# Optimization experiments

Measured on AMD Instinct MI355X. Metric: run time of the kernel, lower is better.

Reference implementation:

```python
import jax, jax.numpy as jnp
import numpy as np

N_EMBD = 768
N_HEAD = 12
HEAD_DIM = N_EMBD // N_HEAD
B, T = 2, 2048
EPS = 1e-5


def setup_inputs() -> dict:
    key = jax.random.key(0)
    ks = jax.random.split(key, 16)
    s = 0.02
    return {
        "x": jax.random.normal(ks[0], (B, T, N_EMBD), dtype=jnp.float32),
        "ln1_g": jnp.ones((N_EMBD,), jnp.float32),
        "ln1_b": jnp.zeros((N_EMBD,), jnp.float32),
        "W_attn": jax.random.normal(ks[1], (N_EMBD, 3 * N_EMBD), jnp.float32) * s,
        "b_attn": jnp.zeros((3 * N_EMBD,), jnp.float32),
        "W_cproj": jax.random.normal(ks[2], (N_EMBD, N_EMBD), jnp.float32) * s,
        "b_cproj": jnp.zeros((N_EMBD,), jnp.float32),
        "ln2_g": jnp.ones((N_EMBD,), jnp.float32),
        "ln2_b": jnp.zeros((N_EMBD,), jnp.float32),
        "W_fc": jax.random.normal(ks[3], (N_EMBD, 4 * N_EMBD), jnp.float32) * s,
        "b_fc": jnp.zeros((4 * N_EMBD,), jnp.float32),
        "W_mproj": jax.random.normal(ks[4], (4 * N_EMBD, N_EMBD), jnp.float32) * s,
        "b_mproj": jnp.zeros((N_EMBD,), jnp.float32),
    }


def _layernorm(x, g, b):
    mu = jnp.mean(x, axis=-1, keepdims=True)
    var = jnp.mean(jnp.square(x - mu), axis=-1, keepdims=True)
    return (x - mu) * jax.lax.rsqrt(var + EPS) * g + b


def _attention(h, W_attn, b_attn, W_cproj, b_cproj):
    Bx, Tx, C = h.shape
    qkv = h @ W_attn + b_attn  # [B, T, 3C]
    q, k, v = jnp.split(qkv, 3, axis=-1)
    # [B, H, T, D]
    def split_heads(t):
        return t.reshape(Bx, Tx, N_HEAD, HEAD_DIM).transpose(0, 2, 1, 3)
    q, k, v = split_heads(q), split_heads(k), split_heads(v)
    att = jnp.einsum("bhqd,bhkd->bhqk", q, k) / np.sqrt(HEAD_DIM).astype(np.float32)
    causal = jnp.tril(jnp.ones((Tx, Tx), dtype=bool))
    att = jnp.where(causal, att, jnp.float32(-jnp.inf))
    att = jax.nn.softmax(att, axis=-1)
    y = jnp.einsum("bhqk,bhkd->bhqd", att, v)
    y = y.transpose(0, 2, 1, 3).reshape(Bx, Tx, C)
    return y @ W_cproj + b_cproj


def _mlp(h, W_fc, b_fc, W_mproj, b_mproj):
    return jax.nn.gelu(h @ W_fc + b_fc, approximate=False) @ W_mproj + b_mproj


def reference(x, ln1_g, ln1_b, W_attn, b_attn, W_cproj, b_cproj,
              ln2_g, ln2_b, W_fc, b_fc, W_mproj, b_mproj):
    x = x + _attention(_layernorm(x, ln1_g, ln1_b), W_attn, b_attn, W_cproj, b_cproj)
    x = x + _mlp(_layernorm(x, ln2_g, ln2_b), W_fc, b_fc, W_mproj, b_mproj)
    return x
```

## Files before the change

### kernel.cpp

```cpp
#include <hip/hip_runtime.h>
#include <cstdint>
#include <cstddef>

#define B_ 2
#define T_ 2048
#define C_ 768
#define H_ 12
#define D_ 64

typedef __attribute__((ext_vector_type(8))) short s16x8;
typedef __attribute__((ext_vector_type(4))) float fx4;

static __device__ __forceinline__ unsigned short f2bf(float f) {
  unsigned u = __builtin_bit_cast(unsigned, f);
  unsigned r = u + 0x7fffu + ((u >> 16) & 1u);
  return (unsigned short)(r >> 16);
}
static __device__ __forceinline__ unsigned short f2bf_trunc(float f) {
  return (unsigned short)(__builtin_bit_cast(unsigned, f) >> 16);
}

static __device__ __forceinline__ void glds16(const unsigned short* g, unsigned short* l) {
  __builtin_amdgcn_global_load_lds(
      (const __attribute__((address_space(1))) void*)(g),
      (__attribute__((address_space(3))) void*)(l), 16, 0, 0);
}

__global__ __launch_bounds__(256) void prep(
    const float* __restrict__ Wattn, const float* __restrict__ Wcproj,
    const float* __restrict__ Wfc, const float* __restrict__ Wmproj,
    unsigned short* __restrict__ WattnT, unsigned short* __restrict__ WcprojT,
    unsigned short* __restrict__ WfcT, unsigned short* __restrict__ WmprojT,
    const float* __restrict__ X, const float* __restrict__ g,
    const float* __restrict__ bb, unsigned short* __restrict__ O) {
  __shared__ float tile[32][33];
  __shared__ float ps[8];
  int bid = blockIdx.x, tid = threadIdx.x;
  if (bid < 6912) {
    const float* W; unsigned short* Wt; int R, C, idx;
    if (bid < 1728)      { W = Wattn;  Wt = WattnT;  R = 768;  C = 2304; idx = bid; }
    else if (bid < 2304) { W = Wcproj; Wt = WcprojT; R = 768;  C = 768;  idx = bid - 1728; }
    else if (bid < 4608) { W = Wfc;    Wt = WfcT;    R = 768;  C = 3072; idx = bid - 2304; }
    else                 { W = Wmproj; Wt = WmprojT; R = 3072; C = 768;  idx = bid - 4608; }
    int ct = C >> 5;
    int c0 = (idx % ct) * 32, r0 = (idx / ct) * 32;
    int tx = tid & 31, ty = tid >> 5;
#pragma unroll
    for (int i = 0; i < 4; ++i)
      tile[ty + i * 8][tx] = W[(size_t)(r0 + ty + i * 8) * C + (c0 + tx)];
    __syncthreads();
#pragma unroll
    for (int i = 0; i < 4; ++i)
      Wt[(size_t)(c0 + ty + i * 8) * R + (r0 + tx)] = f2bf(tile[tx][ty + i * 8]);
  } else {
    int row = bid - 6912;
    const float* xr = X + (size_t)row * C_;
    float v0 = xr[tid], v1 = xr[tid + 256], v2 = xr[tid + 512];
    float s = v0 + v1 + v2;
    float s2 = v0 * v0 + v1 * v1 + v2 * v2;
#pragma unroll
    for (int off = 1; off < 64; off <<= 1) {
      s += __shfl_xor(s, off);
      s2 += __shfl_xor(s2, off);
    }
    int wv = tid >> 6;
    if ((tid & 63) == 0) { ps[wv] = s; ps[wv + 4] = s2; }
    __syncthreads();
    s = ps[0] + ps[1] + ps[2] + ps[3];
    s2 = ps[4] + ps[5] + ps[6] + ps[7];
    float mu = s * (1.f / C_);
    float var = s2 * (1.f / C_) - mu * mu;
    float rstd = rsqrtf(var + 1e-5f);
    unsigned short* orow = O + (size_t)row * C_;
    orow[tid]       = f2bf((v0 - mu) * rstd * g[tid]       + bb[tid]);
    orow[tid + 256] = f2bf((v1 - mu) * rstd * g[tid + 256] + bb[tid + 256]);
    orow[tid + 512] = f2bf((v2 - mu) * rstd * g[tid + 512] + bb[tid + 512]);
  }
}

__global__ __launch_bounds__(256) void layernorm_bf16(
    const float* __restrict__ X, const float* __restrict__ g,
    const float* __restrict__ bb, unsigned short* __restrict__ O) {
  int row = blockIdx.x, tid = threadIdx.x;
  const float* xr = X + (size_t)row * C_;
  float v0 = xr[tid], v1 = xr[tid + 256], v2 = xr[tid + 512];
  float s = v0 + v1 + v2;
  float s2 = v0 * v0 + v1 * v1 + v2 * v2;
#pragma unroll
  for (int off = 1; off < 64; off <<= 1) {
    s += __shfl_xor(s, off);
    s2 += __shfl_xor(s2, off);
  }
  __shared__ float ps[8];
  int wv = tid >> 6;
  if ((tid & 63) == 0) { ps[wv] = s; ps[wv + 4] = s2; }
  __syncthreads();
  s = ps[0] + ps[1] + ps[2] + ps[3];
  s2 = ps[4] + ps[5] + ps[6] + ps[7];
  float mu = s * (1.f / C_);
  float var = s2 * (1.f / C_) - mu * mu;
  float rstd = rsqrtf(var + 1e-5f);
  unsigned short* orow = O + (size_t)row * C_;
  orow[tid]       = f2bf((v0 - mu) * rstd * g[tid]       + bb[tid]);
  orow[tid + 256] = f2bf((v1 - mu) * rstd * g[tid + 256] + bb[tid + 256]);
  orow[tid + 512] = f2bf((v2 - mu) * rstd * g[tid + 512] + bb[tid + 512]);
}

__global__ __launch_bounds__(256) void reduce_out(
    const float* __restrict__ x1, const float* __restrict__ P,
    const float* __restrict__ bias, float* __restrict__ out) {
  int idx = blockIdx.x * 256 + threadIdx.x;
  float4 a = ((const float4*)x1)[idx];
  float4 p = ((const float4*)P)[idx];
  float4 q = ((const float4*)(P + (size_t)4096 * 768))[idx];
  float4 b = ((const float4*)bias)[idx % 192];
  float4 o;
  o.x = a.x + p.x + q.x + b.x;
  o.y = a.y + p.y + q.y + b.y;
  o.z = a.z + p.z + q.z + b.z;
  o.w = a.w + p.w + q.w + b.w;
  ((float4*)out)[idx] = o;
}

template <int BM, int BN, int BK, int MODE>
__global__ __launch_bounds__(256) void gemm_db(
    const unsigned short* __restrict__ A, const unsigned short* __restrict__ Bt,
    const float* __restrict__ bias, const float* __restrict__ resid,
    float* __restrict__ outF, unsigned short* __restrict__ outB,
    unsigned short* __restrict__ qO, unsigned short* __restrict__ kO,
    unsigned short* __restrict__ vtO, int M, int N, int K, int KC) {
  constexpr int AT = BM / 32;
  constexpr int BT = BN / 32;
  constexpr int KS = BK / 32;
  constexpr int ACH = BM * BK / 8;
  constexpr int BCH = BN * BK / 8;
  constexpr int ASZ = BM * BK, BSZ = BN * BK;
  constexpr bool SWIZ = (BK == 64);
  __shared__ __align__(16) unsigned short As[2 * ASZ];
  __shared__ __align__(16) unsigned short Bs[2 * BSZ];
  int tid = threadIdx.x;
  int wv = tid >> 6, lane = tid & 63, quad = lane >> 4, l15 = lane & 15;
  int wm = wv >> 1, wn = wv & 1;
  int m0, n0;
  if (MODE == 1 || MODE == 3) { m0 = blockIdx.x * BM; n0 = blockIdx.y * BN; }
  else                        { n0 = blockIdx.x * BN; m0 = blockIdx.y * BM; }
  const unsigned short* Ak = A + (size_t)blockIdx.z * KC;
  const unsigned short* Bk = Bt + (size_t)blockIdx.z * KC;
  fx4 acc[AT][BT];
#pragma unroll
  for (int i = 0; i < AT; ++i)
#pragma unroll
    for (int j = 0; j < BT; ++j) acc[i][j] = fx4{0.f, 0.f, 0.f, 0.f};

  int nk = KC / BK;
#pragma unroll
  for (int i0 = 0; i0 < ACH; i0 += 256)
    if (ACH - i0 >= 256 || tid < ACH - i0) {
      int e = (i0 + tid) * 8;
      int row = e / BK, col = e & (BK - 1);
      if (SWIZ) col = (((col >> 3) ^ (row & 7)) << 3);
      glds16(&Ak[(size_t)(m0 + row) * K + col], &As[(i0 + (tid & ~63)) * 8]);
    }
#pragma unroll
  for (int i0 = 0; i0 < BCH; i0 += 256)
    if (BCH - i0 >= 256 || tid < BCH - i0) {
      int e = (i0 + tid) * 8;
      int row = e / BK, col = e & (BK - 1);
      if (SWIZ) col = (((col >> 3) ^ (row & 7)) << 3);
      glds16(&Bk[(size_t)(n0 + row) * K + col], &Bs[(i0 + (tid & ~63)) * 8]);
    }
  for (int kt = 0; kt < nk; ++kt) {
    int cur = kt & 1;
    __syncthreads();
    if (kt + 1 < nk) {
      int kb = (kt + 1) * BK;
      int nxt = cur ^ 1;
#pragma unroll
      for (int i0 = 0; i0 < ACH; i0 += 256)
        if (ACH - i0 >= 256 || tid < ACH - i0) {
          int e = (i0 + tid) * 8;
          int row = e / BK, col = e & (BK - 1);
          if (SWIZ) col = (((col >> 3) ^ (row & 7)) << 3);
          glds16(&Ak[(size_t)(m0 + row) * K + kb + col],
                 &As[nxt * ASZ + (i0 + (tid & ~63)) * 8]);
        }
#pragma unroll
      for (int i0 = 0; i0 < BCH; i0 += 256)
        if (BCH - i0 >= 256 || tid < BCH - i0) {
          int e = (i0 + tid) * 8;
          int row = e / BK, col = e & (BK - 1);
          if (SWIZ) col = (((col >> 3) ^ (row & 7)) << 3);
          glds16(&Bk[(size_t)(n0 + row) * K + kb + col],
                 &Bs[nxt * BSZ + (i0 + (tid & ~63)) * 8]);
        }
    }
#pragma unroll
    for (int ks = 0; ks < KS; ++ks) {
      s16x8 af[AT], bf[BT];
#pragma unroll
      for (int mt = 0; mt < AT; ++mt) {
        int r = wm * (BM / 2) + mt * 16 + l15;
        int c = ks * 32 + quad * 8;
        if (SWIZ) c = (((c >> 3) ^ (r & 7)) << 3);
        af[mt] = *(const s16x8*)&As[cur * ASZ + r * BK + c];
      }
#pragma unroll
      for (int nt = 0; nt < BT; ++nt) {
        int r = wn * (BN / 2) + nt * 16 + l15;
        int c = ks * 32 + quad * 8;
        if (SWIZ) c = (((c >> 3) ^ (r & 7)) << 3);
        bf[nt] = *(const s16x8*)&Bs[cur * BSZ + r * BK + c];
      }
#pragma unroll
      for (int mt = 0; mt < AT; ++mt)
#pragma unroll
        for (int nt = 0; nt < BT; ++nt)
          acc[mt][nt] = __builtin_amdgcn_mfma_f32_16x16x32_bf16(af[mt], bf[nt], acc[mt][nt], 0, 0, 0);
    }
  }

#pragma unroll
  for (int mt = 0; mt < AT; ++mt)
#pragma unroll
    for (int nt = 0; nt < BT; ++nt) {
      int mb = m0 + wm * (BM / 2) + mt * 16 + quad * 4;
      int n = n0 + wn * (BN / 2) + nt * 16 + l15;
      if (MODE == 0) {
        int which = n / C_;
        int within = n - which * C_;
        int hd = within >> 6, d = within & 63;
        int bbx = mb >> 11, t = mb & 2047;
        size_t bh = (size_t)(bbx * H_ + hd);
        float b = bias[n];
        if (which == 2) {
          unsigned v01 = (unsigned)f2bf(acc[mt][nt][0] + b) |
                         ((unsigned)f2bf(acc[mt][nt][1] + b) << 16);
          unsigned v23 = (unsigned)f2bf(acc[mt][nt][2] + b) |
                         ((unsigned)f2bf(acc[mt][nt][3] + b) << 16);
          *(uint2*)&vtO[(bh * D_ + d) * T_ + t] = uint2{v01, v23};
        } else {
          unsigned short* dst = (which == 0) ? qO : kO;
#pragma unroll
          for (int r = 0; r < 4; ++r)
            dst[(bh * T_ + t + r) * D_ + d] = f2bf(acc[mt][nt][r] + b);
        }
      } else if (MODE == 1) {
#pragma unroll
        for (int r = 0; r < 4; ++r) {
          int m = mb + r;
          float v = acc[mt][nt][r] + bias[n];
          outF[(size_t)m * N + n] = resid[(size_t)m * N + n] + v;
        }
      } else if (MODE == 3) {
        float* P = outF + (size_t)blockIdx.z * M * N;
#pragma unroll
        for (int r = 0; r < 4; ++r)
          P[(size_t)(mb + r) * N + n] = acc[mt][nt][r];
      } else {
#pragma unroll
        for (int r = 0; r < 4; ++r) {
          int m = mb + r;
          float v = acc[mt][nt][r] + bias[n];
          float gl = 0.5f * v * (1.f + erff(v * 0.70710678118654752f));
          outB[(size_t)m * N + n] = f2bf(gl);
        }
      }
    }
}

__global__ __launch_bounds__(256) void attn_fused(
    const unsigned short* __restrict__ Q, const unsigned short* __restrict__ Kg,
    const unsigned short* __restrict__ Vt, unsigned short* __restrict__ Y) {
  __shared__ __align__(16) unsigned short Ks[64 * 72];
  __shared__ __align__(16) unsigned short Vs[64 * 72];
  __shared__ __align__(16) unsigned short Ps[4][16 * 72];
  int tid = threadIdx.x;
  int wv = tid >> 6, lane = tid & 63, quad = lane >> 4, l15 = lane & 15;
  int l = blockIdx.x;
  int w = l >> 8, c = l & 255;
  int i = c & 31;
  int bh = w * 8 + (c >> 5);
  int qt;
  if (w == 0)      qt = i;
  else if (w == 1) qt = (i + 16) & 31;
  else             qt = (i < 16) ? (30 - 2 * i) : (63 - 2 * i);
  int bbx = bh / H_, hh = bh - bbx * H_;
  int q0 = qt * 64;
  size_t base = (size_t)bh * T_ * D_;
  size_t vbase = (size_t)bh * D_ * T_;
  int qrow = q0 + wv * 16 + l15;
  s16x8 qf0 = *(const s16x8*)&Q[base + (size_t)qrow * D_ + quad * 8];
  s16x8 qf1 = *(const s16x8*)&Q[base + (size_t)qrow * D_ + 32 + quad * 8];
  float lsum[4];
  fx4 oacc[4];
#pragma unroll
  for (int t = 0; t < 4; ++t) {
    lsum[t] = 0.f;
    oacc[t] = fx4{0.f, 0.f, 0.f, 0.f};
  }
  int r0s = tid >> 3;
  int c8 = (tid & 7) * 8;
  uint4 ka, kc, va, vc;
  {
    ka = *(const uint4*)&Kg[base + (size_t)r0s * D_ + c8];
    kc = *(const uint4*)&Kg[base + (size_t)(r0s + 32) * D_ + c8];
    va = *(const uint4*)&Vt[vbase + (size_t)r0s * T_ + c8];
    vc = *(const uint4*)&Vt[vbase + (size_t)(r0s + 32) * T_ + c8];
  }
  for (int kb = 0; kb <= qt; ++kb) {
    int k0 = kb * 64;
    __syncthreads();
    *(uint4*)&Ks[r0s * 72 + c8] = ka;
    *(uint4*)&Ks[(r0s + 32) * 72 + c8] = kc;
    *(uint4*)&Vs[r0s * 72 + c8] = va;
    *(uint4*)&Vs[(r0s + 32) * 72 + c8] = vc;
    __syncthreads();
    if (kb < qt) {
      int kn = k0 + 64;
      ka = *(const uint4*)&Kg[base + (size_t)(kn + r0s) * D_ + c8];
      kc = *(const uint4*)&Kg[base + (size_t)(kn + r0s + 32) * D_ + c8];
      va = *(const uint4*)&Vt[vbase + (size_t)r0s * T_ + kn + c8];
      vc = *(const uint4*)&Vt[vbase + (size_t)(r0s + 32) * T_ + kn + c8];
    }
    fx4 sc[4];
#pragma unroll
    for (int nt = 0; nt < 4; ++nt) {
      sc[nt] = fx4{0.f, 0.f, 0.f, 0.f};
      s16x8 kf0 = *(const s16x8*)&Ks[(nt * 16 + l15) * 72 + quad * 8];
      s16x8 kf1 = *(const s16x8*)&Ks[(nt * 16 + l15) * 72 + 32 + quad * 8];
      sc[nt] = __builtin_amdgcn_mfma_f32_16x16x32_bf16(qf0, kf0, sc[nt], 0, 0, 0);
      sc[nt] = __builtin_amdgcn_mfma_f32_16x16x32_bf16(qf1, kf1, sc[nt], 0, 0, 0);
    }
    bool diag = (kb == qt);
    unsigned short* pw = &Ps[wv][0];
#pragma unroll
    for (int nt = 0; nt < 4; ++nt)
#pragma unroll
      for (int r = 0; r < 4; ++r) {
        float p;
        if (diag && (k0 + nt * 16 + l15) > (q0 + wv * 16 + quad * 4 + r)) {
          p = 0.f;
        } else {
          p = __expf(sc[nt][r] * 0.125f);
        }
        lsum[r] += p;
        pw[(quad * 4 + r) * 72 + nt * 16 + l15] = f2bf_trunc(p);
      }
    s16x8 pa0 = *(const s16x8*)&pw[l15 * 72 + quad * 8];
    s16x8 pa1 = *(const s16x8*)&pw[l15 * 72 + 32 + quad * 8];
#pragma unroll
    for (int nt = 0; nt < 4; ++nt) {
      s16x8 vf0 = *(const s16x8*)&Vs[(nt * 16 + l15) * 72 + quad * 8];
      s16x8 vf1 = *(const s16x8*)&Vs[(nt * 16 + l15) * 72 + 32 + quad * 8];
      oacc[nt] = __builtin_amdgcn_mfma_f32_16x16x32_bf16(pa0, vf0, oacc[nt], 0, 0, 0);
      oacc[nt] = __builtin_amdgcn_mfma_f32_16x16x32_bf16(pa1, vf1, oacc[nt], 0, 0, 0);
    }
  }
#pragma unroll
  for (int r = 0; r < 4; ++r) {
#pragma unroll
    for (int off = 1; off < 16; off <<= 1) lsum[r] += __shfl_xor(lsum[r], off);
  }
#pragma unroll
  for (int nt = 0; nt < 4; ++nt)
#pragma unroll
    for (int r = 0; r < 4; ++r) {
      float o = oacc[nt][r] / lsum[r];
      int token = bbx * T_ + q0 + wv * 16 + quad * 4 + r;
      Y[(size_t)token * C_ + hh * D_ + nt * 16 + l15] = f2bf(o);
    }
}

extern "C" void kernel_launch(void* const* d_in, const int* in_sizes, int n_in,
                              void* d_out, int out_size, void* d_ws, size_t ws_size,
                              hipStream_t stream) {
  const float* x      = (const float*)d_in[0];
  const float* ln1g   = (const float*)d_in[1];
  const float* ln1b   = (const float*)d_in[2];
  const float* Wattn  = (const float*)d_in[3];
  const float* battn  = (const float*)d_in[4];
  const float* Wcproj = (const float*)d_in[5];
  const float* bcproj = (const float*)d_in[6];
  const float* ln2g   = (const float*)d_in[7];
  const float* ln2b   = (const float*)d_in[8];
  const float* Wfc    = (const float*)d_in[9];
  const float* bfc    = (const float*)d_in[10];
  const float* Wmproj = (const float*)d_in[11];
  const float* bmproj = (const float*)d_in[12];
  float* out = (float*)d_out;
  char* ws = (char*)d_ws;

  unsigned short* WattnT  = (unsigned short*)(ws + 0);
  unsigned short* WcprojT = (unsigned short*)(ws + 3538944);
  unsigned short* WfcT    = (unsigned short*)(ws + 4718592);
  unsigned short* WmprojT = (unsigned short*)(ws + 9437184);
  unsigned short* hbuf    = (unsigned short*)(ws + 14155776);
  unsigned short* Qb      = (unsigned short*)(ws + 20447232);
  unsigned short* Kb      = (unsigned short*)(ws + 26738688);
  unsigned short* Vtb     = (unsigned short*)(ws + 33030144);
  unsigned short* Yb      = (unsigned short*)(ws + 39321600);
  float*          x1      = (float*)(ws + 45613056);
  unsigned short* Ab      = (unsigned short*)(ws + 58195968);
  float*          Pbuf    = (float*)(ws + 20447232);

  prep<<<11008, 256, 0, stream>>>(Wattn, Wcproj, Wfc, Wmproj,
                                  WattnT, WcprojT, WfcT, WmprojT,
                                  x, ln1g, ln1b, hbuf);

  gemm_db<128, 96, 32, 0><<<dim3(24, 32), 256, 0, stream>>>(
      hbuf, WattnT, battn, nullptr, nullptr, nullptr, Qb, Kb, Vtb,
      4096, 2304, 768, 768);

  attn_fused<<<768, 256, 0, stream>>>(Qb, Kb, Vtb, Yb);

  gemm_db<128, 64, 64, 1><<<dim3(32, 12), 256, 0, stream>>>(
      Yb, WcprojT, bcproj, x, x1, nullptr, nullptr, nullptr, nullptr,
      4096, 768, 768, 768);

  layernorm_bf16<<<4096, 256, 0, stream>>>(x1, ln2g, ln2b, hbuf);

  gemm_db<128, 128, 32, 2><<<dim3(24, 32), 256, 0, stream>>>(
      hbuf, WfcT, bfc, nullptr, nullptr, Ab, nullptr, nullptr, nullptr,
      4096, 3072, 768, 768);

  gemm_db<128, 64, 64, 3><<<dim3(32, 12, 2), 256, 0, stream>>>(
      Ab, WmprojT, bmproj, nullptr, Pbuf, nullptr, nullptr, nullptr, nullptr,
      4096, 768, 3072, 1536);

  reduce_out<<<3072, 256, 0, stream>>>(x1, Pbuf, bmproj, out);
}
```

Baseline: 259.3 us.

## Widen attention key tiles to 128, swizzle BK=32 GEMM LDS, fast GELU

The attention kernel now processes 128 keys per iteration instead of 64, which halves the number of barriers and loop iterations per query tile. The causal mask is now applied unconditionally, so the second half of a diagonal block does wasted compute. The GEMM adds an XOR swizzle for BK=32 tiles to reduce LDS bank conflicts. The exact erf GELU is replaced by a tanh-style sigmoid approximation with truncated bf16 rounding, which changes numerics slightly.

```diff
diff --git a/kernel.cpp b/kernel.cpp
--- a/kernel.cpp
+++ b/kernel.cpp
@@ -136,6 +136,7 @@
   constexpr int BCH = BN * BK / 8;
   constexpr int ASZ = BM * BK, BSZ = BN * BK;
   constexpr bool SWIZ = (BK == 64);
+  constexpr bool SWIZ32 = (BK == 32);
   __shared__ __align__(16) unsigned short As[2 * ASZ];
   __shared__ __align__(16) unsigned short Bs[2 * BSZ];
   int tid = threadIdx.x;
@@ -157,17 +158,19 @@
   for (int i0 = 0; i0 < ACH; i0 += 256)
     if (ACH - i0 >= 256 || tid < ACH - i0) {
       int e = (i0 + tid) * 8;
-      int row = e / BK, col = e & (BK - 1);
-      if (SWIZ) col = (((col >> 3) ^ (row & 7)) << 3);
-      glds16(&Ak[(size_t)(m0 + row) * K + col], &As[(i0 + (tid & ~63)) * 8]);
+      int row = e / BK, cg = (e & (BK - 1)) >> 3;
+      if (SWIZ) cg ^= (row & 7);
+      if (SWIZ32) cg ^= ((row >> 1) & 3);
+      glds16(&Ak[(size_t)(m0 + row) * K + (cg << 3)], &As[(i0 + (tid & ~63)) * 8]);
     }
 #pragma unroll
   for (int i0 = 0; i0 < BCH; i0 += 256)
     if (BCH - i0 >= 256 || tid < BCH - i0) {
       int e = (i0 + tid) * 8;
-      int row = e / BK, col = e & (BK - 1);
-      if (SWIZ) col = (((col >> 3) ^ (row & 7)) << 3);
-      glds16(&Bk[(size_t)(n0 + row) * K + col], &Bs[(i0 + (tid & ~63)) * 8]);
+      int row = e / BK, cg = (e & (BK - 1)) >> 3;
+      if (SWIZ) cg ^= (row & 7);
+      if (SWIZ32) cg ^= ((row >> 1) & 3);
+      glds16(&Bk[(size_t)(n0 + row) * K + (cg << 3)], &Bs[(i0 + (tid & ~63)) * 8]);
     }
   for (int kt = 0; kt < nk; ++kt) {
     int cur = kt & 1;
@@ -179,18 +182,20 @@
       for (int i0 = 0; i0 < ACH; i0 += 256)
         if (ACH - i0 >= 256 || tid < ACH - i0) {
           int e = (i0 + tid) * 8;
-          int row = e / BK, col = e & (BK - 1);
-          if (SWIZ) col = (((col >> 3) ^ (row & 7)) << 3);
-          glds16(&Ak[(size_t)(m0 + row) * K + kb + col],
+          int row = e / BK, cg = (e & (BK - 1)) >> 3;
+          if (SWIZ) cg ^= (row & 7);
+          if (SWIZ32) cg ^= ((row >> 1) & 3);
+          glds16(&Ak[(size_t)(m0 + row) * K + kb + (cg << 3)],
                  &As[nxt * ASZ + (i0 + (tid & ~63)) * 8]);
         }
 #pragma unroll
       for (int i0 = 0; i0 < BCH; i0 += 256)
         if (BCH - i0 >= 256 || tid < BCH - i0) {
           int e = (i0 + tid) * 8;
-          int row = e / BK, col = e & (BK - 1);
-          if (SWIZ) col = (((col >> 3) ^ (row & 7)) << 3);
-          glds16(&Bk[(size_t)(n0 + row) * K + kb + col],
+          int row = e / BK, cg = (e & (BK - 1)) >> 3;
+          if (SWIZ) cg ^= (row & 7);
+          if (SWIZ32) cg ^= ((row >> 1) & 3);
+          glds16(&Bk[(size_t)(n0 + row) * K + kb + (cg << 3)],
                  &Bs[nxt * BSZ + (i0 + (tid & ~63)) * 8]);
         }
     }
@@ -200,16 +205,18 @@
 #pragma unroll
       for (int mt = 0; mt < AT; ++mt) {
         int r = wm * (BM / 2) + mt * 16 + l15;
-        int c = ks * 32 + quad * 8;
-        if (SWIZ) c = (((c >> 3) ^ (r & 7)) << 3);
-        af[mt] = *(const s16x8*)&As[cur * ASZ + r * BK + c];
+        int cg = (ks * 32 + quad * 8) >> 3;
+        if (SWIZ) cg ^= (r & 7);
+        if (SWIZ32) cg ^= ((r >> 1) & 3);
+        af[mt] = *(const s16x8*)&As[cur * ASZ + r * BK + (cg << 3)];
       }
 #pragma unroll
       for (int nt = 0; nt < BT; ++nt) {
         int r = wn * (BN / 2) + nt * 16 + l15;
-        int c = ks * 32 + quad * 8;
-        if (SWIZ) c = (((c >> 3) ^ (r & 7)) << 3);
-        bf[nt] = *(const s16x8*)&Bs[cur * BSZ + r * BK + c];
+        int cg = (ks * 32 + quad * 8) >> 3;
+        if (SWIZ) cg ^= (r & 7);
+        if (SWIZ32) cg ^= ((r >> 1) & 3);
+        bf[nt] = *(const s16x8*)&Bs[cur * BSZ + r * BK + (cg << 3)];
       }
 #pragma unroll
       for (int mt = 0; mt < AT; ++mt)
@@ -261,8 +268,10 @@
         for (int r = 0; r < 4; ++r) {
           int m = mb + r;
           float v = acc[mt][nt][r] + bias[n];
-          float gl = 0.5f * v * (1.f + erff(v * 0.70710678118654752f));
-          outB[(size_t)m * N + n] = f2bf(gl);
+          float w2 = v * v;
+          float u2 = v * (-1.5957691216f - 0.0713548163f * w2);
+          float gl = v * __frcp_rn(1.f + __expf(u2));
+          outB[(size_t)m * N + n] = f2bf_trunc(gl);
         }
       }
     }
@@ -271,9 +280,9 @@
 __global__ __launch_bounds__(256) void attn_fused(
     const unsigned short* __restrict__ Q, const unsigned short* __restrict__ Kg,
     const unsigned short* __restrict__ Vt, unsigned short* __restrict__ Y) {
-  __shared__ __align__(16) unsigned short Ks[64 * 72];
-  __shared__ __align__(16) unsigned short Vs[64 * 72];
-  __shared__ __align__(16) unsigned short Ps[4][16 * 72];
+  __shared__ __align__(16) unsigned short Ks[128 * 72];
+  __shared__ __align__(16) unsigned short Vs[64 * 136];
+  __shared__ __align__(16) unsigned short Ps[4][16 * 136];
   int tid = threadIdx.x;
   int wv = tid >> 6, lane = tid & 63, quad = lane >> 4, l15 = lane & 15;
   int l = blockIdx.x;
@@ -298,62 +307,78 @@
     lsum[t] = 0.f;
     oacc[t] = fx4{0.f, 0.f, 0.f, 0.f};
   }
+  int nDbl = (qt >> 1) + 1;
   int r0s = tid >> 3;
   int c8 = (tid & 7) * 8;
-  uint4 ka, kc, va, vc;
+  uint4 ka0, ka1, ka2, ka3, va0, va1, va2, va3;
   {
-    ka = *(const uint4*)&Kg[base + (size_t)r0s * D_ + c8];
-    kc = *(const uint4*)&Kg[base + (size_t)(r0s + 32) * D_ + c8];
-    va = *(const uint4*)&Vt[vbase + (size_t)r0s * T_ + c8];
-    vc = *(const uint4*)&Vt[vbase + (size_t)(r0s + 32) * T_ + c8];
-  }
-  for (int kb = 0; kb <= qt; ++kb) {
-    int k0 = kb * 64;
+    const unsigned short* Kp = Kg + base;
+    ka0 = *(const uint4*)&Kp[(size_t)r0s * D_ + c8];
+    ka1 = *(const uint4*)&Kp[(size_t)(r0s + 32) * D_ + c8];
+    ka2 = *(const uint4*)&Kp[(size_t)(r0s + 64) * D_ + c8];
+    ka3 = *(const uint4*)&Kp[(size_t)(r0s + 96) * D_ + c8];
+    const unsigned short* Vp = Vt + vbase;
+    va0 = *(const uint4*)&Vp[(size_t)r0s * T_ + c8];
+    va1 = *(const uint4*)&Vp[(size_t)r0s * T_ + 64 + c8];
+    va2 = *(const uint4*)&Vp[(size_t)(r0s + 32) * T_ + c8];
+    va3 = *(const uint4*)&Vp[(size_t)(r0s + 32) * T_ + 64 + c8];
+  }
+  unsigned short* pw = &Ps[wv][0];
+  for (int kb = 0; kb < nDbl; ++kb) {
+    int k0 = kb * 128;
     __syncthreads();
-    *(uint4*)&Ks[r0s * 72 + c8] = ka;
-    *(uint4*)&Ks[(r0s + 32) * 72 + c8] = kc;
-    *(uint4*)&Vs[r0s * 72 + c8] = va;
-    *(uint4*)&Vs[(r0s + 32) * 72 + c8] = vc;
+    *(uint4*)&Ks[r0s * 72 + c8] = ka0;
+    *(uint4*)&Ks[(r0s + 32) * 72 + c8] = ka1;
+    *(uint4*)&Ks[(r0s + 64) * 72 + c8] = ka2;
+    *(uint4*)&Ks[(r0s + 96) * 72 + c8] = ka3;
+    *(uint4*)&Vs[r0s * 136 + c8] = va0;
+    *(uint4*)&Vs[r0s * 136 + 64 + c8] = va1;
+    *(uint4*)&Vs[(r0s + 32) * 136 + c8] = va2;
+    *(uint4*)&Vs[(r0s + 32) * 136 + 64 + c8] = va3;
     __syncthreads();
-    if (kb < qt) {
-      int kn = k0 + 64;
-      ka = *(const uint4*)&Kg[base + (size_t)(kn + r0s) * D_ + c8];
-      kc = *(const uint4*)&Kg[base + (size_t)(kn + r0s + 32) * D_ + c8];
-      va = *(const uint4*)&Vt[vbase + (size_t)r0s * T_ + kn + c8];
-      vc = *(const uint4*)&Vt[vbase + (size_t)(r0s + 32) * T_ + kn + c8];
-    }
-    fx4 sc[4];
-#pragma unroll
-    for (int nt = 0; nt < 4; ++nt) {
+    if (kb + 1 < nDbl) {
+      int kn = k0 + 128;
+      const unsigned short* Kp = Kg + base + (size_t)kn * D_;
+      ka0 = *(const uint4*)&Kp[(size_t)r0s * D_ + c8];
+      ka1 = *(const uint4*)&Kp[(size_t)(r0s + 32) * D_ + c8];
+      ka2 = *(const uint4*)&Kp[(size_t)(r0s + 64) * D_ + c8];
+      ka3 = *(const uint4*)&Kp[(size_t)(r0s + 96) * D_ + c8];
+      const unsigned short* Vp = Vt + vbase + kn;
+      va0 = *(const uint4*)&Vp[(size_t)r0s * T_ + c8];
+      va1 = *(const uint4*)&Vp[(size_t)r0s * T_ + 64 + c8];
+      va2 = *(const uint4*)&Vp[(size_t)(r0s + 32) * T_ + c8];
+      va3 = *(const uint4*)&Vp[(size_t)(r0s + 32) * T_ + 64 + c8];
+    }
+    fx4 sc[8];
+#pragma unroll
+    for (int nt = 0; nt < 8; ++nt) {
       sc[nt] = fx4{0.f, 0.f, 0.f, 0.f};
       s16x8 kf0 = *(const s16x8*)&Ks[(nt * 16 + l15) * 72 + quad * 8];
       s16x8 kf1 = *(const s16x8*)&Ks[(nt * 16 + l15) * 72 + 32 + quad * 8];
       sc[nt] = __builtin_amdgcn_mfma_f32_16x16x32_bf16(qf0, kf0, sc[nt], 0, 0, 0);
       sc[nt] = __builtin_amdgcn_mfma_f32_16x16x32_bf16(qf1, kf1, sc[nt], 0, 0, 0);
     }
-    bool diag = (kb == qt);
-    unsigned short* pw = &Ps[wv][0];
-#pragma unroll
-    for (int nt = 0; nt < 4; ++nt)
+#pragma unroll
+    for (int nt = 0; nt < 8; ++nt)
 #pragma unroll
       for (int r = 0; r < 4; ++r) {
-        float p;
-        if (diag && (k0 + nt * 16 + l15) > (q0 + wv * 16 + quad * 4 + r)) {
-          p = 0.f;
-        } else {
-          p = __expf(sc[nt][r] * 0.125f);
-        }
+        int key = k0 + nt * 16 + l15;
+        int row = q0 + wv * 16 + quad * 4 + r;
+        float p = (key > row) ? 0.f : __expf(sc[nt][r] * 0.125f);
         lsum[r] += p;
-        pw[(quad * 4 + r) * 72 + nt * 16 + l15] = f2bf_trunc(p);
+        pw[(quad * 4 + r) * 136 + nt * 16 + l15] = f2bf_trunc(p);
       }
-    s16x8 pa0 = *(const s16x8*)&pw[l15 * 72 + quad * 8];
-    s16x8 pa1 = *(const s16x8*)&pw[l15 * 72 + 32 + quad * 8];
+    s16x8 pa[4];
+#pragma unroll
+    for (int ch = 0; ch < 4; ++ch)
+      pa[ch] = *(const s16x8*)&pw[l15 * 136 + ch * 32 + quad * 8];
 #pragma unroll
     for (int nt = 0; nt < 4; ++nt) {
-      s16x8 vf0 = *(const s16x8*)&Vs[(nt * 16 + l15) * 72 + quad * 8];
-      s16x8 vf1 = *(const s16x8*)&Vs[(nt * 16 + l15) * 72 + 32 + quad * 8];
-      oacc[nt] = __builtin_amdgcn_mfma_f32_16x16x32_bf16(pa0, vf0, oacc[nt], 0, 0, 0);
-      oacc[nt] = __builtin_amdgcn_mfma_f32_16x16x32_bf16(pa1, vf1, oacc[nt], 0, 0, 0);
+#pragma unroll
+      for (int ch = 0; ch < 4; ++ch) {
+        s16x8 vf = *(const s16x8*)&Vs[(nt * 16 + l15) * 136 + ch * 32 + quad * 8];
+        oacc[nt] = __builtin_amdgcn_mfma_f32_16x16x32_bf16(pa[ch], vf, oacc[nt], 0, 0, 0);
+      }
     }
   }
 #pragma unroll
```

New measurement: 265.6 us. 1.02x slower.
